# Kernel tuning notes

Measured on AMD Instinct MI355X. Metric: run time of the kernel, lower is better.

## Reference

```python
import jax, jax.numpy as jnp
import numpy as np

SIZE = 1 << 24          # number of leaves (power of two, so bound == SIZE)
BOUND = 1 << 24         # padded power-of-two bound, as in SegmentTree.__init__
LOG2_BOUND = 24         # tree depth; traversal runs exactly this many steps
BATCH = 65536           # number of sampled prefix values


def setup_inputs() -> dict:
    key = jax.random.key(0)
    k1, k2 = jax.random.split(key)
    # leaf priorities must be non-negative (docstring warning for prefix-sum query)
    leaf = jax.random.uniform(k1, (SIZE,), dtype=jnp.float32)
    # fractions in [0,1); scaled by the root sum inside reference
    value_frac = jax.random.uniform(k2, (BATCH,), dtype=jnp.float32)
    return {"leaf": leaf, "value_frac": value_frac}


def _build_tree(leaf):
    """Bottom-up sums: heap layout, tree[1] = root, leaves at tree[BOUND:2*BOUND].
    Equivalent to repeated _setitem parent updates, done level-by-level (vectorized)."""
    levels = [leaf]
    lvl = leaf
    for _ in range(LOG2_BOUND):
        lvl = lvl.reshape(-1, 2).sum(axis=1)  # parent = left + right
        levels.append(lvl)
    # index 0 is an unused dummy slot (heap is 1-indexed)
    return jnp.concatenate([jnp.zeros((1,), leaf.dtype)] + levels[::-1])


def reference(leaf, value_frac):
    tree = _build_tree(leaf)
    # sampled prefix-sum targets in [0, root_sum)
    value = value_frac * tree[1]
    # faithful translation of _get_prefix_sum_idx: root-to-leaf binary descent.
    # The torch while-loop runs exactly log2(bound) iterations (index: 1 -> bound),
    # so a static Python loop is the jit-friendly equivalent.
    index = jnp.ones(value.shape, dtype=jnp.int32)  # 2*BOUND < 2^31, int32 safe
    for _ in range(LOG2_BOUND):
        index = index * 2
        lsons = tree[index]            # left-child subtree sums (gather)
        direct = lsons < value         # go right if left subtree too small
        value = value - lsons * direct
        index = index + direct
    index = index - BOUND              # convert heap position to leaf index
    priorities = leaf[index]           # priority of the sampled leaves
    return index, priorities
```

## Files before the change

### kernel.cpp

```cpp
#include <hip/hip_runtime.h>


#define LEAVES_LG 24
#define BATCH_N   65536

#define OFF_ROOT 0
#define OFF_L21  4
#define OFF_L18  16
#define OFF_L15  80
#define OFF_L12  592
#define OFF_L9   4688
#define OFF_L6   37456
#define OFF_L3   299600

__device__ __forceinline__ float sum8_exact(float x0, float x1, float x2, float x3,
                                            float x4, float x5, float x6, float x7) {
    return ((x0 + x1) + (x2 + x3)) + ((x4 + x5) + (x6 + x7));
}

__global__ __launch_bounds__(256) void build_lo(const float* __restrict__ leaf,
                                                float* __restrict__ ws) {
    __shared__ float sm[256];
    __shared__ float sm2[32];
    const int t = threadIdx.x;
    const size_t gid = (size_t)blockIdx.x * 256 + t;
    const float4* lv = reinterpret_cast<const float4*>(leaf) + gid * 2;
    float4 a = lv[0];
    float4 b = lv[1];
    float s3 = sum8_exact(a.x, a.y, a.z, a.w, b.x, b.y, b.z, b.w);
    ws[OFF_L3 + gid] = s3;
    sm[t] = s3;
    __syncthreads();
    if (t < 32) {
        float s6 = sum8_exact(sm[8*t+0], sm[8*t+1], sm[8*t+2], sm[8*t+3],
                              sm[8*t+4], sm[8*t+5], sm[8*t+6], sm[8*t+7]);
        ws[OFF_L6 + (size_t)blockIdx.x * 32 + t] = s6;
        sm2[t] = s6;
    }
    __syncthreads();
    if (t < 4) {
        float s9 = sum8_exact(sm2[8*t+0], sm2[8*t+1], sm2[8*t+2], sm2[8*t+3],
                              sm2[8*t+4], sm2[8*t+5], sm2[8*t+6], sm2[8*t+7]);
        ws[OFF_L9 + (size_t)blockIdx.x * 4 + t] = s9;
    }
}

__global__ __launch_bounds__(256) void build_mid(float* __restrict__ ws) {
    __shared__ float sm[256];
    __shared__ float sm2[32];
    const int t = threadIdx.x;
    const int b = blockIdx.x;
    const float4* in = reinterpret_cast<const float4*>(ws + OFF_L9 + (size_t)b * 2048) + (size_t)t * 2;
    float4 x = in[0];
    float4 y = in[1];
    float s12 = sum8_exact(x.x, x.y, x.z, x.w, y.x, y.y, y.z, y.w);
    ws[OFF_L12 + (size_t)b * 256 + t] = s12;
    sm[t] = s12;
    __syncthreads();
    if (t < 32) {
        float s15 = sum8_exact(sm[8*t+0], sm[8*t+1], sm[8*t+2], sm[8*t+3],
                               sm[8*t+4], sm[8*t+5], sm[8*t+6], sm[8*t+7]);
        ws[OFF_L15 + (size_t)b * 32 + t] = s15;
        sm2[t] = s15;
    }
    __syncthreads();
    if (t < 4) {
        float s18 = sum8_exact(sm2[8*t+0], sm2[8*t+1], sm2[8*t+2], sm2[8*t+3],
                               sm2[8*t+4], sm2[8*t+5], sm2[8*t+6], sm2[8*t+7]);
        ws[OFF_L18 + (size_t)b * 4 + t] = s18;
    }
}

__global__ __launch_bounds__(64) void build_top(float* __restrict__ ws) {
    __shared__ float sm[8];
    const int t = threadIdx.x;
    if (t < 8) {
        const float* in = ws + OFF_L18 + t * 8;
        float s21 = sum8_exact(in[0], in[1], in[2], in[3], in[4], in[5], in[6], in[7]);
        ws[OFF_L21 + t] = s21;
        sm[t] = s21;
    }
    __syncthreads();
    if (t == 0) {
        ws[OFF_ROOT] = sum8_exact(sm[0], sm[1], sm[2], sm[3], sm[4], sm[5], sm[6], sm[7]);
    }
}

__device__ __forceinline__ void step8(const float* __restrict__ base, int& p, float& v,
                                      float& picked) {
    const float4* q = reinterpret_cast<const float4*>(base + (size_t)p * 8);
    float4 x = q[0];
    float4 y = q[1];
    float n0 = x.x + x.y;
    float n2 = y.x + y.y;
    float t2 = n0 + (x.z + x.w);
    int ia = t2 < v;
    if (ia) v -= t2;
    float pn = ia ? n2 : n0;
    int ib = pn < v;
    if (ib) v -= pn;
    float ce = ia ? (ib ? y.z : y.x) : (ib ? x.z : x.x);
    float co = ia ? (ib ? y.w : y.y) : (ib ? x.w : x.y);
    int ic = ce < v;
    if (ic) v -= ce;
    picked = ic ? co : ce;
    p = p * 8 + ia * 4 + ib * 2 + ic;
}

__global__ __launch_bounds__(256) void descend(const float* __restrict__ leaf,
                                               const float* __restrict__ frac,
                                               const float* __restrict__ ws,
                                               float* __restrict__ out) {
    const int tid = blockIdx.x * 256 + threadIdx.x;
    float v = frac[tid] * ws[OFF_ROOT];
    int p = 0;
    float picked = 0.0f;
    step8(ws + OFF_L21, p, v, picked);
    step8(ws + OFF_L18, p, v, picked);
    step8(ws + OFF_L15, p, v, picked);
    step8(ws + OFF_L12, p, v, picked);
    step8(ws + OFF_L9,  p, v, picked);
    step8(ws + OFF_L6,  p, v, picked);
    step8(ws + OFF_L3,  p, v, picked);
    step8(leaf,         p, v, picked);
    out[tid] = (float)p;
    out[BATCH_N + tid] = picked;
}

extern "C" void kernel_launch(void* const* d_in, const int* in_sizes, int n_in,
                              void* d_out, int out_size, void* d_ws, size_t ws_size,
                              hipStream_t stream) {
    const float* leaf = (const float*)d_in[0];
    const float* frac = (const float*)d_in[1];
    float* out = (float*)d_out;
    float* ws  = (float*)d_ws;

    hipLaunchKernelGGL(build_lo,  dim3(8192), dim3(256), 0, stream, leaf, ws);
    hipLaunchKernelGGL(build_mid, dim3(16),   dim3(256), 0, stream, ws);
    hipLaunchKernelGGL(build_top, dim3(1),    dim3(64),  0, stream, ws);
    hipLaunchKernelGGL(descend,   dim3(256),  dim3(256), 0, stream, leaf, frac, ws, out);
}
```

Measured before the change: 100.8 us.

## Switch tree to radix-16 stored levels and drop one build kernel

Stores only every fourth tree level instead of every third, so each build thread reduces 16 leaves and the descent loads 64-byte nodes of 16 children, taking 4 binary decisions per step over 6 steps instead of 8. The build shrinks from three kernels to two, removing a launch and a dependent pass. The intended savings are fewer dependent gather rounds in the latency-bound descent and less workspace written. In exchange each gather is twice as wide and each step does more in-register additions and selects, with the same pairwise summation order as before.

```diff
diff --git a/kernel.cpp b/kernel.cpp
--- a/kernel.cpp
+++ b/kernel.cpp
@@ -1,110 +1,97 @@
 #include <hip/hip_runtime.h>
 
 
-#define LEAVES_LG 24
-#define BATCH_N   65536
+#define BATCH_N 65536
 
 #define OFF_ROOT 0
-#define OFF_L21  4
-#define OFF_L18  16
-#define OFF_L15  80
-#define OFF_L12  592
-#define OFF_L9   4688
-#define OFF_L6   37456
-#define OFF_L3   299600
+#define OFF_A 16
+#define OFF_B 32
+#define OFF_C 288
+#define OFF_D 4384
+#define OFF_E 69920
 
-__device__ __forceinline__ float sum8_exact(float x0, float x1, float x2, float x3,
-                                            float x4, float x5, float x6, float x7) {
-    return ((x0 + x1) + (x2 + x3)) + ((x4 + x5) + (x6 + x7));
+__device__ __forceinline__ float sum16_exact(float4 A, float4 B, float4 C, float4 D) {
+    float n0 = A.x + A.y, n1 = A.z + A.w, n2 = B.x + B.y, n3 = B.z + B.w;
+    float n4 = C.x + C.y, n5 = C.z + C.w, n6 = D.x + D.y, n7 = D.z + D.w;
+    float m0 = n0 + n1, m1 = n2 + n3, m2 = n4 + n5, m3 = n6 + n7;
+    return (m0 + m1) + (m2 + m3);
+}
+
+__device__ __forceinline__ float sum16_exact_s(const float* __restrict__ x) {
+    float n0 = x[0] + x[1],  n1 = x[2] + x[3],  n2 = x[4] + x[5],  n3 = x[6] + x[7];
+    float n4 = x[8] + x[9],  n5 = x[10] + x[11], n6 = x[12] + x[13], n7 = x[14] + x[15];
+    float m0 = n0 + n1, m1 = n2 + n3, m2 = n4 + n5, m3 = n6 + n7;
+    return (m0 + m1) + (m2 + m3);
 }
 
 __global__ __launch_bounds__(256) void build_lo(const float* __restrict__ leaf,
                                                 float* __restrict__ ws) {
-    __shared__ float sm[256];
-    __shared__ float sm2[32];
+    __shared__ float smE[256];
+    __shared__ float smD[16];
     const int t = threadIdx.x;
-    const size_t gid = (size_t)blockIdx.x * 256 + t;
-    const float4* lv = reinterpret_cast<const float4*>(leaf) + gid * 2;
-    float4 a = lv[0];
-    float4 b = lv[1];
-    float s3 = sum8_exact(a.x, a.y, a.z, a.w, b.x, b.y, b.z, b.w);
-    ws[OFF_L3 + gid] = s3;
-    sm[t] = s3;
+    const int b = blockIdx.x;
+    const size_t gid = (size_t)b * 256 + t;
+    const float4* q = reinterpret_cast<const float4*>(leaf) + gid * 4;
+    float4 A = q[0], Bv = q[1], Cv = q[2], Dv = q[3];
+    float e = sum16_exact(A, Bv, Cv, Dv);
+    ws[OFF_E + gid] = e;
+    smE[t] = e;
     __syncthreads();
-    if (t < 32) {
-        float s6 = sum8_exact(sm[8*t+0], sm[8*t+1], sm[8*t+2], sm[8*t+3],
-                              sm[8*t+4], sm[8*t+5], sm[8*t+6], sm[8*t+7]);
-        ws[OFF_L6 + (size_t)blockIdx.x * 32 + t] = s6;
-        sm2[t] = s6;
+    if (t < 16) {
+        float d = sum16_exact_s(&smE[16 * t]);
+        ws[OFF_D + (size_t)b * 16 + t] = d;
+        smD[t] = d;
     }
     __syncthreads();
-    if (t < 4) {
-        float s9 = sum8_exact(sm2[8*t+0], sm2[8*t+1], sm2[8*t+2], sm2[8*t+3],
-                              sm2[8*t+4], sm2[8*t+5], sm2[8*t+6], sm2[8*t+7]);
-        ws[OFF_L9 + (size_t)blockIdx.x * 4 + t] = s9;
+    if (t == 0) {
+        ws[OFF_C + b] = sum16_exact_s(smD);
     }
 }
 
-__global__ __launch_bounds__(256) void build_mid(float* __restrict__ ws) {
-    __shared__ float sm[256];
-    __shared__ float sm2[32];
+__global__ __launch_bounds__(256) void build_top(float* __restrict__ ws) {
+    __shared__ float smB[256];
+    __shared__ float smA[16];
     const int t = threadIdx.x;
-    const int b = blockIdx.x;
-    const float4* in = reinterpret_cast<const float4*>(ws + OFF_L9 + (size_t)b * 2048) + (size_t)t * 2;
-    float4 x = in[0];
-    float4 y = in[1];
-    float s12 = sum8_exact(x.x, x.y, x.z, x.w, y.x, y.y, y.z, y.w);
-    ws[OFF_L12 + (size_t)b * 256 + t] = s12;
-    sm[t] = s12;
+    const float4* q = reinterpret_cast<const float4*>(ws + OFF_C) + (size_t)t * 4;
+    float4 A = q[0], Bv = q[1], Cv = q[2], Dv = q[3];
+    float bnode = sum16_exact(A, Bv, Cv, Dv);
+    ws[OFF_B + t] = bnode;
+    smB[t] = bnode;
     __syncthreads();
-    if (t < 32) {
-        float s15 = sum8_exact(sm[8*t+0], sm[8*t+1], sm[8*t+2], sm[8*t+3],
-                               sm[8*t+4], sm[8*t+5], sm[8*t+6], sm[8*t+7]);
-        ws[OFF_L15 + (size_t)b * 32 + t] = s15;
-        sm2[t] = s15;
+    if (t < 16) {
+        float anode = sum16_exact_s(&smB[16 * t]);
+        ws[OFF_A + t] = anode;
+        smA[t] = anode;
     }
     __syncthreads();
-    if (t < 4) {
-        float s18 = sum8_exact(sm2[8*t+0], sm2[8*t+1], sm2[8*t+2], sm2[8*t+3],
-                               sm2[8*t+4], sm2[8*t+5], sm2[8*t+6], sm2[8*t+7]);
-        ws[OFF_L18 + (size_t)b * 4 + t] = s18;
+    if (t == 0) {
+        ws[OFF_ROOT] = sum16_exact_s(smA);
     }
 }
 
-__global__ __launch_bounds__(64) void build_top(float* __restrict__ ws) {
-    __shared__ float sm[8];
-    const int t = threadIdx.x;
-    if (t < 8) {
-        const float* in = ws + OFF_L18 + t * 8;
-        float s21 = sum8_exact(in[0], in[1], in[2], in[3], in[4], in[5], in[6], in[7]);
-        ws[OFF_L21 + t] = s21;
-        sm[t] = s21;
-    }
-    __syncthreads();
-    if (t == 0) {
-        ws[OFF_ROOT] = sum8_exact(sm[0], sm[1], sm[2], sm[3], sm[4], sm[5], sm[6], sm[7]);
-    }
-}
+__device__ __forceinline__ void step16(const float* __restrict__ base, int& p, float& v,
+                                       float& picked) {
+    const float4* q = reinterpret_cast<const float4*>(base + (size_t)p * 16);
+    float4 A = q[0], B = q[1], C = q[2], D = q[3];
+    float n0 = A.x + A.y, n2 = B.x + B.y, n4 = C.x + C.y, n6 = D.x + D.y;
+    float m0 = n0 + (A.z + A.w);
+    float m2 = n4 + (C.z + C.w);
+    float t0 = m0 + (n2 + (B.z + B.w));
 
-__device__ __forceinline__ void step8(const float* __restrict__ base, int& p, float& v,
-                                      float& picked) {
-    const float4* q = reinterpret_cast<const float4*>(base + (size_t)p * 8);
-    float4 x = q[0];
-    float4 y = q[1];
-    float n0 = x.x + x.y;
-    float n2 = y.x + y.y;
-    float t2 = n0 + (x.z + x.w);
-    int ia = t2 < v;
-    if (ia) v -= t2;
-    float pn = ia ? n2 : n0;
-    int ib = pn < v;
-    if (ib) v -= pn;
-    float ce = ia ? (ib ? y.z : y.x) : (ib ? x.z : x.x);
-    float co = ia ? (ib ? y.w : y.y) : (ib ? x.w : x.y);
-    int ic = ce < v;
-    if (ic) v -= ce;
-    picked = ic ? co : ce;
-    p = p * 8 + ia * 4 + ib * 2 + ic;
+    int ia = t0 < v;  if (ia) v -= t0;
+    float mm = ia ? m2 : m0;
+    int ib = mm < v;  if (ib) v -= mm;
+    float nn = ia ? (ib ? n6 : n4) : (ib ? n2 : n0);
+    int ic = nn < v;  if (ic) v -= nn;
+    float se0 = ia ? C.x : A.x, se1 = ia ? C.z : A.z;
+    float se2 = ia ? D.x : B.x, se3 = ia ? D.z : B.z;
+    float so0 = ia ? C.y : A.y, so1 = ia ? C.w : A.w;
+    float so2 = ia ? D.y : B.y, so3 = ia ? D.w : B.w;
+    float ce = ic ? (ib ? se3 : se1) : (ib ? se2 : se0);
+    float co = ic ? (ib ? so3 : so1) : (ib ? so2 : so0);
+    int id = ce < v;  if (id) v -= ce;
+    picked = id ? co : ce;
+    p = p * 16 + ia * 8 + ib * 4 + ic * 2 + id;
 }
 
 __global__ __launch_bounds__(256) void descend(const float* __restrict__ leaf,
@@ -115,14 +102,12 @@
     float v = frac[tid] * ws[OFF_ROOT];
     int p = 0;
     float picked = 0.0f;
-    step8(ws + OFF_L21, p, v, picked);
-    step8(ws + OFF_L18, p, v, picked);
-    step8(ws + OFF_L15, p, v, picked);
-    step8(ws + OFF_L12, p, v, picked);
-    step8(ws + OFF_L9,  p, v, picked);
-    step8(ws + OFF_L6,  p, v, picked);
-    step8(ws + OFF_L3,  p, v, picked);
-    step8(leaf,         p, v, picked);
+    step16(ws + OFF_A, p, v, picked);
+    step16(ws + OFF_B, p, v, picked);
+    step16(ws + OFF_C, p, v, picked);
+    step16(ws + OFF_D, p, v, picked);
+    step16(ws + OFF_E, p, v, picked);
+    step16(leaf,       p, v, picked);
     out[tid] = (float)p;
     out[BATCH_N + tid] = picked;
 }
@@ -135,8 +120,7 @@
     float* out = (float*)d_out;
     float* ws  = (float*)d_ws;
 
-    hipLaunchKernelGGL(build_lo,  dim3(8192), dim3(256), 0, stream, leaf, ws);
-    hipLaunchKernelGGL(build_mid, dim3(16),   dim3(256), 0, stream, ws);
-    hipLaunchKernelGGL(build_top, dim3(1),    dim3(64),  0, stream, ws);
+    hipLaunchKernelGGL(build_lo,  dim3(4096), dim3(256), 0, stream, leaf, ws);
+    hipLaunchKernelGGL(build_top, dim3(1),    dim3(256), 0, stream, ws);
     hipLaunchKernelGGL(descend,   dim3(256),  dim3(256), 0, stream, leaf, frac, ws, out);
 }
```

Result: faster. 97.98 us (median of 2 runs) (-2.8%).
